# Performance work log

Measured on AMD Instinct MI355X. Metric: run time of the kernel, lower is better.

The kernel has to match this reference:

```python
import jax, jax.numpy as jnp
import numpy as np

N, L, DV, EF = 64, 128, 16, 4
D, H, FF, LC, K, MS = 256, 8, 1024, 3, 6, 16
DK = D // H
NEG = -1e9


def _ln(x, g, b):
    m = x.mean(-1, keepdims=True)
    v = ((x - m) ** 2).mean(-1, keepdims=True)
    return (x - m) / jnp.sqrt(v + 1e-5) * g + b


def setup_inputs() -> dict:
    key = jax.random.key(0)
    ks = jax.random.split(key, 20)
    s = 0.05
    rn = lambda k, sh: jax.random.normal(k, sh, jnp.float32) * s
    return {
        "vehicles": jax.random.normal(ks[0], (N, L, DV), jnp.float32),
        "fleet_edges": jax.random.uniform(ks[1], (N, L, L, EF), jnp.float32),
        "Wproj": rn(ks[2], (DV, D)), "bproj": jnp.zeros((D,), jnp.float32),
        "Wq": rn(ks[3], (LC, D, D)), "Wk": rn(ks[4], (LC, D, D)), "Wv": rn(ks[5], (LC, D, D)),
        "mix1_w": rn(ks[6], (LC, H, 2, MS)), "mix1_b": jnp.zeros((LC, H, MS), jnp.float32),
        "mix2_w": rn(ks[7], (LC, H, MS)), "mix2_b": jnp.zeros((LC, H), jnp.float32),
        "Wo": rn(ks[8], (LC, D, D)), "bo": jnp.zeros((LC, D), jnp.float32),
        "n1_g": jnp.ones((LC, D), jnp.float32), "n1_b": jnp.zeros((LC, D), jnp.float32),
        "ff1_w": rn(ks[9], (LC, D, FF)), "ff1_b": jnp.zeros((LC, FF), jnp.float32),
        "ff2_w": rn(ks[10], (LC, FF, D)), "ff2_b": jnp.zeros((LC, D), jnp.float32),
        "n2_g": jnp.ones((LC, D), jnp.float32), "n2_b": jnp.zeros((LC, D), jnp.float32),
    }


def _forward(vehicles, fleet_edges, Wproj, bproj, Wq, Wk, Wv, mix1_w, mix1_b,
             mix2_w, mix2_b, Wo, bo, n1_g, n1_b, ff1_w, ff1_b, ff2_w, ff2_b, n2_g, n2_b):
    h = vehicles @ Wproj + bproj                      # (N, L, D)
    dist = fleet_edges[..., 0]                        # (N, L, L)
    cost = dist
    # kNN mask: keep K smallest distances per row; mask==True -> blocked
    _, knn_idx = jax.lax.top_k(-dist, K)              # (N, L, K)
    nbr = jnp.any(jax.nn.one_hot(knn_idx, L, dtype=bool), axis=2)  # (N, L, L)
    mask = ~nbr
    row_fully_masked = mask.all(-1)                   # (N, L)
    inv_sqrt_dk = 1.0 / np.sqrt(DK).astype(np.float32)
    for i in range(LC):
        q = (h @ Wq[i]).reshape(N, L, H, DK).transpose(0, 2, 1, 3)
        k_ = (h @ Wk[i]).reshape(N, L, H, DK).transpose(0, 2, 1, 3)
        v = (h @ Wv[i]).reshape(N, L, H, DK).transpose(0, 2, 1, 3)
        dot = jnp.einsum('nhrd,nhcd->nhrc', q, k_) * inv_sqrt_dk      # (N,H,L,L)
        cost_b = jnp.broadcast_to(cost[:, None], (N, H, L, L))
        two = jnp.stack([dot, cost_b], axis=-1)                        # (N,H,L,L,2)
        ms1 = jax.nn.relu(jnp.einsum('nhrct,htm->nhrcm', two, mix1_w[i])
                          + mix1_b[i][None, :, None, None, :])         # (N,H,L,L,MS)
        score = jnp.einsum('nhrcm,hm->nhrc', ms1, mix2_w[i]) \
                + mix2_b[i][None, :, None, None]                       # (N,H,L,L)
        score = jnp.where(mask[:, None], NEG, score)
        w = jax.nn.softmax(score, axis=-1)
        att = jnp.einsum('nhrc,nhcd->nhrd', w, v)
        att = att.transpose(0, 2, 1, 3).reshape(N, L, D) @ Wo[i] + bo[i]
        h1 = _ln(h + att, n1_g[i], n1_b[i])
        ff = jax.nn.relu(h1 @ ff1_w[i] + ff1_b[i]) @ ff2_w[i] + ff2_b[i]
        h = _ln(h1 + ff, n2_g[i], n2_b[i])
        # original does h_out[mask] = 0; with kNN k>0 every row keeps k entries,
        # so only fully-masked rows would be zeroed (a no-op here, kept for fidelity)
        h = jnp.where(row_fully_masked[..., None], 0.0, h)
    return h


def reference(vehicles, fleet_edges, Wproj, bproj, Wq, Wk, Wv, mix1_w, mix1_b,
              mix2_w, mix2_b, Wo, bo, n1_g, n1_b, ff1_w, ff1_b, ff2_w, ff2_b, n2_g, n2_b):
    return _forward(vehicles, fleet_edges, Wproj, bproj, Wq, Wk, Wv, mix1_w, mix1_b,
                    mix2_w, mix2_b, Wo, bo, n1_g, n1_b, ff1_w, ff1_b, ff2_w, ff2_b, n2_g, n2_b)
```

## Files before the change

kernel.cpp:

```cpp
#include <hip/hip_runtime.h>
#include <math.h>

#define NB 64
#define LL 128
#define DV 16
#define DD 256
#define HH 8
#define DK 32
#define FF 1024
#define LC 3
#define KNN 6
#define MS 16
#define WLS 786432

typedef __attribute__((ext_vector_type(8))) short s16x8;
typedef __attribute__((ext_vector_type(4))) float f32x4;

static __device__ inline unsigned short f2b(float x) {
    union { float f; unsigned int u; } v; v.f = x;
    unsigned int r = (v.u + 0x7FFFu + ((v.u >> 16) & 1u)) >> 16;
    return (unsigned short)r;
}

static __device__ __forceinline__ void glds16(const void* g, void* l) {
    __builtin_amdgcn_global_load_lds(
        (const __attribute__((address_space(1))) void*)g,
        (__attribute__((address_space(3))) void*)l, 16, 0, 0);
}

__global__ __launch_bounds__(256)
void proj2(const float* __restrict__ veh, const float* __restrict__ Wp,
           const float* __restrict__ bp, float* __restrict__ h,
           unsigned short* __restrict__ hb) {
    int m = blockIdx.x * 4 + (threadIdx.x >> 6);
    int l = threadIdx.x & 63;
    int c0 = l * 4;
    const float4* w4 = reinterpret_cast<const float4*>(Wp);
    float4 a = *reinterpret_cast<const float4*>(bp + c0);
    const float* vr = veh + (size_t)m * DV;
#pragma unroll
    for (int t = 0; t < DV; ++t) {
        float vt = vr[t];
        float4 wv = w4[t * 64 + l];
        a.x += vt * wv.x; a.y += vt * wv.y; a.z += vt * wv.z; a.w += vt * wv.w;
    }
    *reinterpret_cast<float4*>(h + (size_t)m * DD + c0) = a;
    ushort4 u; u.x = f2b(a.x); u.y = f2b(a.y); u.z = f2b(a.z); u.w = f2b(a.w);
    *reinterpret_cast<ushort4*>(hb + (size_t)m * DD + c0) = u;
}

__global__ __launch_bounds__(256)
void knn_idx(const float* __restrict__ edges, unsigned long long* __restrict__ idx8) {
    int row = blockIdx.x * 4 + (threadIdx.x >> 6);
    int lane = threadIdx.x & 63;
    const float* dr = edges + (size_t)row * LL * 4;
    float v0 = dr[lane * 4], v1 = dr[(lane + 64) * 4];
    int i0 = lane, i1 = lane + 64;
    unsigned long long packed = 0;
#pragma unroll
    for (int k = 0; k < KNN; ++k) {
        float v; int i;
        if (v1 < v0) { v = v1; i = i1; } else { v = v0; i = i0; }
#pragma unroll
        for (int o = 1; o < 64; o <<= 1) {
            float ov = __shfl_xor(v, o);
            int oi = __shfl_xor(i, o);
            if (ov < v || (ov == v && oi < i)) { v = ov; i = oi; }
        }
        packed |= (unsigned long long)i << (k * 8);
        if (i == i0) v0 = 3.4e38f;
        if (i == i1) v1 = 3.4e38f;
    }
    if (lane == 0) idx8[row] = packed;
}

__global__ __launch_bounds__(256)
void transposeAll(const float* __restrict__ Wq, const float* __restrict__ Wk,
                  const float* __restrict__ Wv, const float* __restrict__ Wo,
                  const float* __restrict__ f1, const float* __restrict__ f2,
                  unsigned short* __restrict__ Wt) {
    int z = blockIdx.y;
    int ll = z / 6, w = z % 6;
    int K = (w == 5) ? FF : DD;
    int N = (w == 4) ? FF : DD;
    const float* src = (w == 0) ? Wq : (w == 1) ? Wk : (w == 2) ? Wv :
                       (w == 3) ? Wo : (w == 4) ? f1 : f2;
    src += (size_t)ll * K * N;
    long off = (w == 4) ? 262144L : (w == 5) ? 524288L : (long)w * 65536L;
    unsigned short* dst = Wt + (size_t)ll * WLS + off;
    int ntx = N >> 5;
    if (blockIdx.x >= ntx * (K >> 5)) return;
    int n0 = (blockIdx.x % ntx) * 32, k0 = (blockIdx.x / ntx) * 32;
    int tx = threadIdx.x & 31, ty = threadIdx.x >> 5;
    __shared__ float T[32][33];
#pragma unroll
    for (int r = 0; r < 4; ++r)
        T[ty + r * 8][tx] = src[(size_t)(k0 + ty + r * 8) * N + n0 + tx];
    __syncthreads();
#pragma unroll
    for (int r = 0; r < 4; ++r)
        dst[(size_t)(n0 + ty + r * 8) * K + k0 + tx] = f2b(T[tx][ty + r * 8]);
}

template <int BM, int BN, int WR, int WC, int MODE>
__global__ __launch_bounds__(256)
void gg(const unsigned short* __restrict__ A, const unsigned short* __restrict__ Bt,
        const float* __restrict__ bias, float* __restrict__ Cf,
        unsigned short* __restrict__ Cb,
        float* __restrict__ Oq, float* __restrict__ Ok, float* __restrict__ Ov,
        int K, int N) {
    constexpr int MI = BM / (WR * 16);
    constexpr int NJ = BN / (WC * 16);
    __shared__ unsigned short As[BM * 32];
    __shared__ unsigned short Bs[BN * 32];
    int tid = threadIdx.x;
    int w = tid >> 6, l = tid & 63;
    int lr = l & 15, lg = l >> 4;
    int wr = w % WR, wc = w / WR;
    int m0 = blockIdx.y * BM, n0 = blockIdx.x * BN;
    int row = tid >> 2, seg = tid & 3;

    f32x4 acc[MI][NJ];
#pragma unroll
    for (int i = 0; i < MI; ++i)
#pragma unroll
        for (int j = 0; j < NJ; ++j) acc[i][j] = (f32x4)(0.f);

    for (int k0 = 0; k0 < K; k0 += 32) {
        __syncthreads();
#pragma unroll
        for (int r = 0; r < BM / 64; ++r)
            glds16(A + (size_t)(m0 + r * 64 + row) * K + k0 + seg * 8,
                   As + r * 2048 + w * 512);
#pragma unroll
        for (int r = 0; r < BN / 64; ++r)
            glds16(Bt + (size_t)(n0 + r * 64 + row) * K + k0 + seg * 8,
                   Bs + r * 2048 + w * 512);
        __syncthreads();
        s16x8 af[MI], bf[NJ];
#pragma unroll
        for (int i = 0; i < MI; ++i)
            af[i] = *reinterpret_cast<const s16x8*>(
                As + (wr * MI * 16 + i * 16 + lr) * 32 + lg * 8);
#pragma unroll
        for (int j = 0; j < NJ; ++j)
            bf[j] = *reinterpret_cast<const s16x8*>(
                Bs + (wc * NJ * 16 + j * 16 + lr) * 32 + lg * 8);
#pragma unroll
        for (int i = 0; i < MI; ++i)
#pragma unroll
            for (int j = 0; j < NJ; ++j)
                acc[i][j] = __builtin_amdgcn_mfma_f32_16x16x32_bf16(af[i], bf[j], acc[i][j], 0, 0, 0);
    }

    if constexpr (MODE == 2) {
        int s = n0 >> 8;
        int nn = blockIdx.y;
        float* dst = (s == 0) ? Oq : (s == 1) ? Ok : Ov;
#pragma unroll
        for (int i = 0; i < MI; ++i)
#pragma unroll
            for (int j = 0; j < NJ; ++j) {
                int cc = (n0 & 255) + j * 16 + lr;
                int hh = cc >> 5, dk = cc & 31;
                int rl = wr * MI * 16 + i * 16 + lg * 4;
                size_t ho = ((size_t)(nn * HH + hh) * LL + rl) * DK + dk;
#pragma unroll
                for (int q = 0; q < 4; ++q)
                    dst[ho + (size_t)q * DK] = acc[i][j][q];
            }
    } else {
#pragma unroll
        for (int i = 0; i < MI; ++i)
#pragma unroll
            for (int j = 0; j < NJ; ++j) {
                int col = n0 + wc * NJ * 16 + j * 16 + lr;
                float bc = bias[col];
#pragma unroll
                for (int q = 0; q < 4; ++q) {
                    int r = m0 + wr * MI * 16 + i * 16 + lg * 4 + q;
                    float v = acc[i][j][q] + bc;
                    if (MODE == 1) {
                        v = fmaxf(v, 0.f);
                        Cb[(size_t)r * N + col] = f2b(v);
                    } else {
                        Cf[(size_t)r * N + col] = v;
                    }
                }
            }
    }
}

__global__ __launch_bounds__(256)
void fattn7(const float* __restrict__ qh, const float* __restrict__ kh,
            const float* __restrict__ vh, const float* __restrict__ edges,
            const unsigned long long* __restrict__ idx8,
            const float* __restrict__ m1w, const float* __restrict__ m1b,
            const float* __restrict__ m2w, const float* __restrict__ m2b,
            unsigned short* __restrict__ attc) {
    int t = blockIdx.x * 256 + threadIdx.x;
    int bh = t >> 7, r = t & 127;
    int n = bh >> 3, hh = bh & 7;
    int hu = __builtin_amdgcn_readfirstlane(hh);
    const float* w0g = m1w + (hu * 2 + 0) * MS;
    const float* w1g = m1w + (hu * 2 + 1) * MS;
    const float* b1g = m1b + hu * MS;
    const float* w2g = m2w + hu * MS;
    float b2v = m2b[hu];
    const float scale = 0.17677669529663687f;

    const float4* qr = reinterpret_cast<const float4*>(qh + ((size_t)bh * LL + r) * DK);
    float4 q[8];
#pragma unroll
    for (int j = 0; j < 8; ++j) q[j] = qr[j];

    unsigned long long pk = idx8[(size_t)n * LL + r];
    const float* kbase = kh + (size_t)bh * LL * DK;
    const float* vbase = vh + (size_t)bh * LL * DK;
    const float* erow = edges + (size_t)(n * LL + r) * LL * 4;

    int col[KNN];
#pragma unroll
    for (int k = 0; k < KNN; ++k) col[k] = (int)((pk >> (k * 8)) & 0xFF);

    float e[KNN];
    float mx = -3.4e38f;
#pragma unroll
    for (int k = 0; k < KNN; ++k) {
        const float4* kr = reinterpret_cast<const float4*>(kbase + (size_t)col[k] * DK);
        float d = 0.f;
#pragma unroll
        for (int j = 0; j < 8; ++j) {
            float4 kv = kr[j];
            d += q[j].x * kv.x + q[j].y * kv.y + q[j].z * kv.z + q[j].w * kv.w;
        }
        d *= scale;
        float cst = erow[col[k] * 4];
        float s = b2v;
#pragma unroll
        for (int m = 0; m < MS; ++m)
            s += fmaxf(d * w0g[m] + cst * w1g[m] + b1g[m], 0.f) * w2g[m];
        e[k] = s;
        mx = fmaxf(mx, s);
    }
    float sum = 0.f;
#pragma unroll
    for (int k = 0; k < KNN; ++k) { e[k] = __expf(e[k] - mx); sum += e[k]; }
    float inv = 1.f / sum;

    float4 att[8];
#pragma unroll
    for (int j = 0; j < 8; ++j) att[j] = make_float4(0.f, 0.f, 0.f, 0.f);
#pragma unroll
    for (int k = 0; k < KNN; ++k) {
        float wgt = e[k] * inv;
        const float4* vr = reinterpret_cast<const float4*>(vbase + (size_t)col[k] * DK);
#pragma unroll
        for (int j = 0; j < 8; ++j) {
            float4 vv = vr[j];
            att[j].x += wgt * vv.x; att[j].y += wgt * vv.y;
            att[j].z += wgt * vv.z; att[j].w += wgt * vv.w;
        }
    }
    unsigned short* dst = attc + ((size_t)(n * LL + r)) * DD + hh * DK;
#pragma unroll
    for (int j = 0; j < 8; ++j) {
        ushort4 u;
        u.x = f2b(att[j].x); u.y = f2b(att[j].y);
        u.z = f2b(att[j].z); u.w = f2b(att[j].w);
        *reinterpret_cast<ushort4*>(dst + j * 4) = u;
    }
}

__global__ __launch_bounds__(256)
void add_ln2(const float* __restrict__ a, const float* __restrict__ b,
             const float* __restrict__ g, const float* __restrict__ be,
             float* __restrict__ out, unsigned short* __restrict__ outb) {
    int m = blockIdx.x * 4 + (threadIdx.x >> 6);
    int l = threadIdx.x & 63;
    size_t off = (size_t)m * DD + l * 4;
    float4 av = *reinterpret_cast<const float4*>(a + off);
    float4 bv = *reinterpret_cast<const float4*>(b + off);
    float4 x = make_float4(av.x + bv.x, av.y + bv.y, av.z + bv.z, av.w + bv.w);
    float s = x.x + x.y + x.z + x.w;
#pragma unroll
    for (int o = 1; o < 64; o <<= 1) s += __shfl_xor(s, o);
    float mean = s * (1.0f / 256.0f);
    float4 d = make_float4(x.x - mean, x.y - mean, x.z - mean, x.w - mean);
    float s2 = d.x * d.x + d.y * d.y + d.z * d.z + d.w * d.w;
#pragma unroll
    for (int o = 1; o < 64; o <<= 1) s2 += __shfl_xor(s2, o);
    float inv = 1.f / sqrtf(s2 * (1.0f / 256.0f) + 1e-5f);
    float4 gv = *reinterpret_cast<const float4*>(g + l * 4);
    float4 ev = *reinterpret_cast<const float4*>(be + l * 4);
    float4 r = make_float4(d.x * inv * gv.x + ev.x, d.y * inv * gv.y + ev.y,
                           d.z * inv * gv.z + ev.z, d.w * inv * gv.w + ev.w);
    *reinterpret_cast<float4*>(out + off) = r;
    ushort4 u; u.x = f2b(r.x); u.y = f2b(r.y); u.z = f2b(r.z); u.w = f2b(r.w);
    *reinterpret_cast<ushort4*>(outb + off) = u;
}

extern "C" void kernel_launch(void* const* d_in, const int* in_sizes, int n_in,
                              void* d_out, int out_size, void* d_ws, size_t ws_size,
                              hipStream_t stream) {
    const float* vehicles = (const float*)d_in[0];
    const float* fleet    = (const float*)d_in[1];
    const float* Wproj    = (const float*)d_in[2];
    const float* bproj    = (const float*)d_in[3];
    const float* Wq       = (const float*)d_in[4];
    const float* Wk       = (const float*)d_in[5];
    const float* Wv       = (const float*)d_in[6];
    const float* m1w      = (const float*)d_in[7];
    const float* m1b      = (const float*)d_in[8];
    const float* m2w      = (const float*)d_in[9];
    const float* m2b      = (const float*)d_in[10];
    const float* Wo       = (const float*)d_in[11];
    const float* bo       = (const float*)d_in[12];
    const float* n1_g     = (const float*)d_in[13];
    const float* n1_b     = (const float*)d_in[14];
    const float* ff1_w    = (const float*)d_in[15];
    const float* ff1_b    = (const float*)d_in[16];
    const float* ff2_w    = (const float*)d_in[17];
    const float* ff2_b    = (const float*)d_in[18];
    const float* n2_g     = (const float*)d_in[19];
    const float* n2_b     = (const float*)d_in[20];

    const size_t MROWS = (size_t)NB * LL;
    const size_t HSZ   = MROWS * DD;

    float* ws = (float*)d_ws;
    float* h   = ws;
    float* tmp = h + HSZ;
    float* qh  = tmp + HSZ;
    float* kh  = qh + HSZ;
    float* vh  = kh + HSZ;
    unsigned short* hb    = (unsigned short*)(vh + HSZ);
    unsigned short* attc  = hb + HSZ;
    unsigned short* ffmid = attc + HSZ;
    unsigned short* Wt    = ffmid + MROWS * FF;
    unsigned long long* idx8 = (unsigned long long*)(Wt + 3 * WLS);

    proj2<<<2048, 256, 0, stream>>>(vehicles, Wproj, bproj, h, hb);
    knn_idx<<<2048, 256, 0, stream>>>(fleet, idx8);
    transposeAll<<<dim3(256, 18), 256, 0, stream>>>(Wq, Wk, Wv, Wo, ff1_w, ff2_w, Wt);

    dim3 gqkv(12, 64);
    dim3 gwo(4, 128);
    dim3 gff1(8, 64);

    for (int i = 0; i < LC; ++i) {
        const unsigned short* wt = Wt + (size_t)i * WLS;

        gg<128, 64, 4, 1, 2><<<gqkv, 256, 0, stream>>>(
            hb, wt, nullptr, nullptr, nullptr, qh, kh, vh, DD, 768);

        fattn7<<<256, 256, 0, stream>>>(
            qh, kh, vh, fleet, idx8,
            m1w + (size_t)i * HH * 2 * MS, m1b + (size_t)i * HH * MS,
            m2w + (size_t)i * HH * MS,     m2b + (size_t)i * HH,
            attc);

        gg<64, 64, 2, 2, 0><<<gwo, 256, 0, stream>>>(
            attc, wt + 196608, bo + (size_t)i * DD, tmp, nullptr,
            nullptr, nullptr, nullptr, DD, DD);
        add_ln2<<<2048, 256, 0, stream>>>(h, tmp, n1_g + (size_t)i * DD,
                                          n1_b + (size_t)i * DD, h, hb);

        gg<128, 128, 2, 2, 1><<<gff1, 256, 0, stream>>>(
            hb, wt + 262144, ff1_b + (size_t)i * FF, nullptr, ffmid,
            nullptr, nullptr, nullptr, DD, FF);

        float* dst = (i == LC - 1) ? (float*)d_out : h;
        gg<64, 64, 2, 2, 0><<<gwo, 256, 0, stream>>>(
            ffmid, wt + 524288, ff2_b + (size_t)i * DD, tmp, nullptr,
            nullptr, nullptr, nullptr, FF, DD);
        add_ln2<<<2048, 256, 0, stream>>>(h, tmp, n2_g + (size_t)i * DD,
                                          n2_b + (size_t)i * DD, dst, hb);
    }
}
```

Before: 261.2 us.

## Fuse output GEMMs with residual LayerNorm and merge prologue kernels

Adds a row-tiled GEMM kernel covering the full 256-wide output per block, so bias, residual add and LayerNorm run in its epilogue. This replaces the separate Wo/FF2 GEMM plus add_ln2 kernels and drops the fp32 tmp buffer round trip. It also merges projection, kNN selection and weight transpose into one launch. The price is that each block streams the whole weight matrix for only 16 rows, with a single-buffered K loop, which lowers GEMM reuse.

Measured after the change: 247.5 us. 1.06x faster.

```diff
diff --git a/kernel.cpp b/kernel.cpp
--- a/kernel.cpp
+++ b/kernel.cpp
@@ -29,84 +29,87 @@
 }
 
 __global__ __launch_bounds__(256)
-void proj2(const float* __restrict__ veh, const float* __restrict__ Wp,
-           const float* __restrict__ bp, float* __restrict__ h,
-           unsigned short* __restrict__ hb) {
-    int m = blockIdx.x * 4 + (threadIdx.x >> 6);
-    int l = threadIdx.x & 63;
-    int c0 = l * 4;
-    const float4* w4 = reinterpret_cast<const float4*>(Wp);
-    float4 a = *reinterpret_cast<const float4*>(bp + c0);
-    const float* vr = veh + (size_t)m * DV;
-#pragma unroll
-    for (int t = 0; t < DV; ++t) {
-        float vt = vr[t];
-        float4 wv = w4[t * 64 + l];
-        a.x += vt * wv.x; a.y += vt * wv.y; a.z += vt * wv.z; a.w += vt * wv.w;
-    }
-    *reinterpret_cast<float4*>(h + (size_t)m * DD + c0) = a;
-    ushort4 u; u.x = f2b(a.x); u.y = f2b(a.y); u.z = f2b(a.z); u.w = f2b(a.w);
-    *reinterpret_cast<ushort4*>(hb + (size_t)m * DD + c0) = u;
-}
-
-__global__ __launch_bounds__(256)
-void knn_idx(const float* __restrict__ edges, unsigned long long* __restrict__ idx8) {
-    int row = blockIdx.x * 4 + (threadIdx.x >> 6);
-    int lane = threadIdx.x & 63;
-    const float* dr = edges + (size_t)row * LL * 4;
-    float v0 = dr[lane * 4], v1 = dr[(lane + 64) * 4];
-    int i0 = lane, i1 = lane + 64;
-    unsigned long long packed = 0;
-#pragma unroll
-    for (int k = 0; k < KNN; ++k) {
-        float v; int i;
-        if (v1 < v0) { v = v1; i = i1; } else { v = v0; i = i0; }
-#pragma unroll
-        for (int o = 1; o < 64; o <<= 1) {
-            float ov = __shfl_xor(v, o);
-            int oi = __shfl_xor(i, o);
-            if (ov < v || (ov == v && oi < i)) { v = ov; i = oi; }
-        }
-        packed |= (unsigned long long)i << (k * 8);
-        if (i == i0) v0 = 3.4e38f;
-        if (i == i1) v1 = 3.4e38f;
-    }
-    if (lane == 0) idx8[row] = packed;
-}
-
-__global__ __launch_bounds__(256)
-void transposeAll(const float* __restrict__ Wq, const float* __restrict__ Wk,
-                  const float* __restrict__ Wv, const float* __restrict__ Wo,
-                  const float* __restrict__ f1, const float* __restrict__ f2,
-                  unsigned short* __restrict__ Wt) {
-    int z = blockIdx.y;
-    int ll = z / 6, w = z % 6;
-    int K = (w == 5) ? FF : DD;
-    int N = (w == 4) ? FF : DD;
-    const float* src = (w == 0) ? Wq : (w == 1) ? Wk : (w == 2) ? Wv :
-                       (w == 3) ? Wo : (w == 4) ? f1 : f2;
-    src += (size_t)ll * K * N;
-    long off = (w == 4) ? 262144L : (w == 5) ? 524288L : (long)w * 65536L;
-    unsigned short* dst = Wt + (size_t)ll * WLS + off;
-    int ntx = N >> 5;
-    if (blockIdx.x >= ntx * (K >> 5)) return;
-    int n0 = (blockIdx.x % ntx) * 32, k0 = (blockIdx.x / ntx) * 32;
-    int tx = threadIdx.x & 31, ty = threadIdx.x >> 5;
-    __shared__ float T[32][33];
-#pragma unroll
-    for (int r = 0; r < 4; ++r)
-        T[ty + r * 8][tx] = src[(size_t)(k0 + ty + r * 8) * N + n0 + tx];
-    __syncthreads();
-#pragma unroll
-    for (int r = 0; r < 4; ++r)
-        dst[(size_t)(n0 + ty + r * 8) * K + k0 + tx] = f2b(T[tx][ty + r * 8]);
+void uber_pre(const float* __restrict__ veh, const float* __restrict__ Wp,
+              const float* __restrict__ bp, float* __restrict__ h,
+              unsigned short* __restrict__ hb,
+              const float* __restrict__ edges, unsigned long long* __restrict__ idx8,
+              const float* __restrict__ Wq, const float* __restrict__ Wk,
+              const float* __restrict__ Wv, const float* __restrict__ Wo,
+              const float* __restrict__ f1, const float* __restrict__ f2,
+              unsigned short* __restrict__ Wt) {
+    int bx = blockIdx.x;
+    if (bx < 2048) {
+        int m = bx * 4 + (threadIdx.x >> 6);
+        int l = threadIdx.x & 63;
+        int c0 = l * 4;
+        const float4* w4 = reinterpret_cast<const float4*>(Wp);
+        float4 a = *reinterpret_cast<const float4*>(bp + c0);
+        const float* vr = veh + (size_t)m * DV;
+#pragma unroll
+        for (int t = 0; t < DV; ++t) {
+            float vt = vr[t];
+            float4 wv = w4[t * 64 + l];
+            a.x += vt * wv.x; a.y += vt * wv.y; a.z += vt * wv.z; a.w += vt * wv.w;
+        }
+        *reinterpret_cast<float4*>(h + (size_t)m * DD + c0) = a;
+        ushort4 u; u.x = f2b(a.x); u.y = f2b(a.y); u.z = f2b(a.z); u.w = f2b(a.w);
+        *reinterpret_cast<ushort4*>(hb + (size_t)m * DD + c0) = u;
+        return;
+    }
+    if (bx < 4096) {
+        int row = (bx - 2048) * 4 + (threadIdx.x >> 6);
+        int lane = threadIdx.x & 63;
+        const float* dr = edges + (size_t)row * LL * 4;
+        float v0 = dr[lane * 4], v1 = dr[(lane + 64) * 4];
+        int i0 = lane, i1 = lane + 64;
+        unsigned long long packed = 0;
+#pragma unroll
+        for (int k = 0; k < KNN; ++k) {
+            float v; int i;
+            if (v1 < v0) { v = v1; i = i1; } else { v = v0; i = i0; }
+#pragma unroll
+            for (int o = 1; o < 64; o <<= 1) {
+                float ov = __shfl_xor(v, o);
+                int oi = __shfl_xor(i, o);
+                if (ov < v || (ov == v && oi < i)) { v = ov; i = oi; }
+            }
+            packed |= (unsigned long long)i << (k * 8);
+            if (i == i0) v0 = 3.4e38f;
+            if (i == i1) v1 = 3.4e38f;
+        }
+        if (lane == 0) idx8[row] = packed;
+        return;
+    }
+    {
+        int t = bx - 4096;
+        int ll = t / 768, r = t % 768;
+        int w, tile, K, N;
+        if (r < 256)      { w = r >> 6; tile = r & 63;  K = DD; N = DD; }
+        else if (r < 512) { w = 4; tile = r - 256;      K = DD; N = FF; }
+        else              { w = 5; tile = r - 512;      K = FF; N = DD; }
+        const float* src = (w == 0) ? Wq : (w == 1) ? Wk : (w == 2) ? Wv :
+                           (w == 3) ? Wo : (w == 4) ? f1 : f2;
+        src += (size_t)ll * K * N;
+        long off = (w == 4) ? 262144L : (w == 5) ? 524288L : (long)w * 65536L;
+        unsigned short* dst = Wt + (size_t)ll * WLS + off;
+        int ntx = N >> 5;
+        int n0 = (tile % ntx) * 32, k0 = (tile / ntx) * 32;
+        int tx = threadIdx.x & 31, ty = threadIdx.x >> 5;
+        __shared__ float T[32][33];
+#pragma unroll
+        for (int rr = 0; rr < 4; ++rr)
+            T[ty + rr * 8][tx] = src[(size_t)(k0 + ty + rr * 8) * N + n0 + tx];
+        __syncthreads();
+#pragma unroll
+        for (int rr = 0; rr < 4; ++rr)
+            dst[(size_t)(n0 + ty + rr * 8) * K + k0 + tx] = f2b(T[tx][ty + rr * 8]);
+    }
 }
 
 template <int BM, int BN, int WR, int WC, int MODE>
 __global__ __launch_bounds__(256)
 void gg(const unsigned short* __restrict__ A, const unsigned short* __restrict__ Bt,
-        const float* __restrict__ bias, float* __restrict__ Cf,
-        unsigned short* __restrict__ Cb,
+        const float* __restrict__ bias, unsigned short* __restrict__ Cb,
         float* __restrict__ Oq, float* __restrict__ Ok, float* __restrict__ Ov,
         int K, int N) {
     constexpr int MI = BM / (WR * 16);
@@ -179,15 +182,113 @@
 #pragma unroll
                 for (int q = 0; q < 4; ++q) {
                     int r = m0 + wr * MI * 16 + i * 16 + lg * 4 + q;
-                    float v = acc[i][j][q] + bc;
-                    if (MODE == 1) {
-                        v = fmaxf(v, 0.f);
-                        Cb[(size_t)r * N + col] = f2b(v);
-                    } else {
-                        Cf[(size_t)r * N + col] = v;
-                    }
+                    float v = fmaxf(acc[i][j][q] + bc, 0.f);
+                    Cb[(size_t)r * N + col] = f2b(v);
                 }
             }
+    }
+}
+
+template <int KK>
+__global__ __launch_bounds__(256)
+void gg_ln(const unsigned short* __restrict__ A, const unsigned short* __restrict__ Bt,
+           const float* __restrict__ bias, const float* __restrict__ res,
+           const float* __restrict__ g, const float* __restrict__ be,
+           float* __restrict__ out, unsigned short* __restrict__ outb) {
+    __shared__ unsigned short As[16 * 32];
+    __shared__ unsigned short Bs[256 * 32];
+    __shared__ float Red[16][4];
+    int tid = threadIdx.x;
+    int w = tid >> 6, l = tid & 63;
+    int lr = l & 15, lg = l >> 4;
+    int m0 = blockIdx.x * 16;
+
+    f32x4 acc[4];
+#pragma unroll
+    for (int j = 0; j < 4; ++j) acc[j] = (f32x4)(0.f);
+
+    for (int k0 = 0; k0 < KK; k0 += 32) {
+        __syncthreads();
+        if (w == 0)
+            glds16(A + (size_t)(m0 + (l >> 2)) * KK + k0 + (l & 3) * 8, As);
+#pragma unroll
+        for (int i = 0; i < 4; ++i) {
+            int idx = w * 4 + i;
+            glds16(Bt + (size_t)(idx * 16 + (l >> 2)) * KK + k0 + (l & 3) * 8,
+                   Bs + idx * 512);
+        }
+        __syncthreads();
+        s16x8 af = *reinterpret_cast<const s16x8*>(As + lr * 32 + lg * 8);
+#pragma unroll
+        for (int j = 0; j < 4; ++j) {
+            s16x8 bf = *reinterpret_cast<const s16x8*>(
+                Bs + (w * 64 + j * 16 + lr) * 32 + lg * 8);
+            acc[j] = __builtin_amdgcn_mfma_f32_16x16x32_bf16(af, bf, acc[j], 0, 0, 0);
+        }
+    }
+
+    float rsum[4] = {0.f, 0.f, 0.f, 0.f};
+#pragma unroll
+    for (int j = 0; j < 4; ++j) {
+        int col = w * 64 + j * 16 + lr;
+        float bc = bias[col];
+#pragma unroll
+        for (int q = 0; q < 4; ++q) {
+            float x = acc[j][q] + bc + res[(size_t)(m0 + lg * 4 + q) * DD + col];
+            acc[j][q] = x;
+            rsum[q] += x;
+        }
+    }
+#pragma unroll
+    for (int q = 0; q < 4; ++q)
+#pragma unroll
+        for (int o = 1; o < 16; o <<= 1) rsum[q] += __shfl_xor(rsum[q], o);
+    __syncthreads();
+    if (lr == 0)
+#pragma unroll
+        for (int q = 0; q < 4; ++q) Red[lg * 4 + q][w] = rsum[q];
+    __syncthreads();
+    float mean[4];
+#pragma unroll
+    for (int q = 0; q < 4; ++q) {
+        int row = lg * 4 + q;
+        mean[q] = (Red[row][0] + Red[row][1] + Red[row][2] + Red[row][3]) * (1.0f / 256.0f);
+    }
+    float ssum[4] = {0.f, 0.f, 0.f, 0.f};
+#pragma unroll
+    for (int j = 0; j < 4; ++j)
+#pragma unroll
+        for (int q = 0; q < 4; ++q) {
+            float d = acc[j][q] - mean[q];
+            ssum[q] += d * d;
+        }
+#pragma unroll
+    for (int q = 0; q < 4; ++q)
+#pragma unroll
+        for (int o = 1; o < 16; o <<= 1) ssum[q] += __shfl_xor(ssum[q], o);
+    __syncthreads();
+    if (lr == 0)
+#pragma unroll
+        for (int q = 0; q < 4; ++q) Red[lg * 4 + q][w] = ssum[q];
+    __syncthreads();
+    float rstd[4];
+#pragma unroll
+    for (int q = 0; q < 4; ++q) {
+        int row = lg * 4 + q;
+        float var = (Red[row][0] + Red[row][1] + Red[row][2] + Red[row][3]) * (1.0f / 256.0f);
+        rstd[q] = 1.0f / sqrtf(var + 1e-5f);
+    }
+#pragma unroll
+    for (int j = 0; j < 4; ++j) {
+        int col = w * 64 + j * 16 + lr;
+        float gc = g[col], bc2 = be[col];
+#pragma unroll
+        for (int q = 0; q < 4; ++q) {
+            size_t off = (size_t)(m0 + lg * 4 + q) * DD + col;
+            float v = (acc[j][q] - mean[q]) * rstd[q] * gc + bc2;
+            out[off] = v;
+            outb[off] = f2b(v);
+        }
     }
 }
 
@@ -270,34 +371,6 @@
         u.z = f2b(att[j].z); u.w = f2b(att[j].w);
         *reinterpret_cast<ushort4*>(dst + j * 4) = u;
     }
-}
-
-__global__ __launch_bounds__(256)
-void add_ln2(const float* __restrict__ a, const float* __restrict__ b,
-             const float* __restrict__ g, const float* __restrict__ be,
-             float* __restrict__ out, unsigned short* __restrict__ outb) {
-    int m = blockIdx.x * 4 + (threadIdx.x >> 6);
-    int l = threadIdx.x & 63;
-    size_t off = (size_t)m * DD + l * 4;
-    float4 av = *reinterpret_cast<const float4*>(a + off);
-    float4 bv = *reinterpret_cast<const float4*>(b + off);
-    float4 x = make_float4(av.x + bv.x, av.y + bv.y, av.z + bv.z, av.w + bv.w);
-    float s = x.x + x.y + x.z + x.w;
-#pragma unroll
-    for (int o = 1; o < 64; o <<= 1) s += __shfl_xor(s, o);
-    float mean = s * (1.0f / 256.0f);
-    float4 d = make_float4(x.x - mean, x.y - mean, x.z - mean, x.w - mean);
-    float s2 = d.x * d.x + d.y * d.y + d.z * d.z + d.w * d.w;
-#pragma unroll
-    for (int o = 1; o < 64; o <<= 1) s2 += __shfl_xor(s2, o);
-    float inv = 1.f / sqrtf(s2 * (1.0f / 256.0f) + 1e-5f);
-    float4 gv = *reinterpret_cast<const float4*>(g + l * 4);
-    float4 ev = *reinterpret_cast<const float4*>(be + l * 4);
-    float4 r = make_float4(d.x * inv * gv.x + ev.x, d.y * inv * gv.y + ev.y,
-                           d.z * inv * gv.z + ev.z, d.w * inv * gv.w + ev.w);
-    *reinterpret_cast<float4*>(out + off) = r;
-    ushort4 u; u.x = f2b(r.x); u.y = f2b(r.y); u.z = f2b(r.z); u.w = f2b(r.w);
-    *reinterpret_cast<ushort4*>(outb + off) = u;
 }
 
 extern "C" void kernel_launch(void* const* d_in, const int* in_sizes, int n_in,
@@ -330,8 +403,7 @@
 
     float* ws = (float*)d_ws;
     float* h   = ws;
-    float* tmp = h + HSZ;
-    float* qh  = tmp + HSZ;
+    float* qh  = h + HSZ;
     float* kh  = qh + HSZ;
     float* vh  = kh + HSZ;
     unsigned short* hb    = (unsigned short*)(vh + HSZ);
@@ -340,19 +412,18 @@
     unsigned short* Wt    = ffmid + MROWS * FF;
     unsigned long long* idx8 = (unsigned long long*)(Wt + 3 * WLS);
 
-    proj2<<<2048, 256, 0, stream>>>(vehicles, Wproj, bproj, h, hb);
-    knn_idx<<<2048, 256, 0, stream>>>(fleet, idx8);
-    transposeAll<<<dim3(256, 18), 256, 0, stream>>>(Wq, Wk, Wv, Wo, ff1_w, ff2_w, Wt);
+    uber_pre<<<6400, 256, 0, stream>>>(vehicles, Wproj, bproj, h, hb,
+                                       fleet, idx8,
+                                       Wq, Wk, Wv, Wo, ff1_w, ff2_w, Wt);
 
     dim3 gqkv(12, 64);
-    dim3 gwo(4, 128);
     dim3 gff1(8, 64);
 
     for (int i = 0; i < LC; ++i) {
         const unsigned short* wt = Wt + (size_t)i * WLS;
 
         gg<128, 64, 4, 1, 2><<<gqkv, 256, 0, stream>>>(
-            hb, wt, nullptr, nullptr, nullptr, qh, kh, vh, DD, 768);
+            hb, wt, nullptr, nullptr, qh, kh, vh, DD, 768);
 
         fattn7<<<256, 256, 0, stream>>>(
             qh, kh, vh, fleet, idx8,
@@ -360,21 +431,17 @@
             m2w + (size_t)i * HH * MS,     m2b + (size_t)i * HH,
             attc);
 
-        gg<64, 64, 2, 2, 0><<<gwo, 256, 0, stream>>>(
-            attc, wt + 196608, bo + (size_t)i * DD, tmp, nullptr,
-            nullptr, nullptr, nullptr, DD, DD);
-        add_ln2<<<2048, 256, 0, stream>>>(h, tmp, n1_g + (size_t)i * DD,
-                                          n1_b + (size_t)i * DD, h, hb);
+        gg_ln<256><<<512, 256, 0, stream>>>(
+            attc, wt + 196608, bo + (size_t)i * DD,
+            h, n1_g + (size_t)i * DD, n1_b + (size_t)i * DD, h, hb);
 
         gg<128, 128, 2, 2, 1><<<gff1, 256, 0, stream>>>(
-            hb, wt + 262144, ff1_b + (size_t)i * FF, nullptr, ffmid,
+            hb, wt + 262144, ff1_b + (size_t)i * FF, ffmid,
             nullptr, nullptr, nullptr, DD, FF);
 
         float* dst = (i == LC - 1) ? (float*)d_out : h;
-        gg<64, 64, 2, 2, 0><<<gwo, 256, 0, stream>>>(
-            ffmid, wt + 524288, ff2_b + (size_t)i * DD, tmp, nullptr,
-            nullptr, nullptr, nullptr, FF, DD);
-        add_ln2<<<2048, 256, 0, stream>>>(h, tmp, n2_g + (size_t)i * DD,
-                                          n2_b + (size_t)i * DD, dst, hb);
-    }
-}
+        gg_ln<1024><<<512, 256, 0, stream>>>(
+            ffmid, wt + 524288, ff2_b + (size_t)i * DD,
+            h, n2_g + (size_t)i * DD, n2_b + (size_t)i * DD, dst, hb);
+    }
+}
```
